# Kernel optimization log

Hardware: AMD Instinct MI355X
Metric: run time of the kernel (lower is better)

The kernel has to match this reference:

```python
import jax, jax.numpy as jnp
import numpy as np

B, H, S, D = 2, 8, 4096, 64

def setup_inputs() -> dict:
    key = jax.random.key(0)
    kq, kk, kv = jax.random.split(key, 3)
    queries = jax.random.normal(kq, (B, H, S, D), dtype=jnp.float32)
    keys = jax.random.normal(kk, (B, H, S, D), dtype=jnp.float32)
    values = jax.random.normal(kv, (B, H, S, D), dtype=jnp.float32)
    adj = jnp.zeros((1,), dtype=jnp.int32)  # unused by the module, kept for signature fidelity
    return {"queries": queries, "keys": keys, "values": values, "adj": adj}

def reference(queries, keys, values, adj):
    # scores: [B,H,S,S]; note the original divides by a hard-coded 16, not sqrt(d)
    scores = jnp.einsum('bhqd,bhkd->bhqk', queries, keys) / 16.0
    attn = jax.nn.softmax(scores, axis=-1)
    # dropout p=0.0 -> identity in eval/deterministic mode
    h = jnp.einsum('bhqk,bhkd->bhqd', attn, values)  # [B,H,S,D]
    # original uses .view (a reshape, NOT a transpose) to (S, B, H, D)
    return jnp.reshape(h, (S, B, H, D))
```

## Files before the change

kernel.cpp:

```cpp
#include <hip/hip_runtime.h>
#include <hip/hip_bf16.h>
#include <math.h>

#define S_LEN 4096
#define D_DIM 64
#define NBH   16
#define QPRE  0.09016844f

typedef __attribute__((ext_vector_type(8))) short bf16x8;
typedef __attribute__((ext_vector_type(4))) float f32x4;
typedef __attribute__((ext_vector_type(4))) __fp16 f16x4;
typedef __attribute__((ext_vector_type(2))) __fp16 f16x2;

__device__ __forceinline__ unsigned int pkbf(float lo, float hi) {
  unsigned int ua = __float_as_uint(lo) + 0x8000u;
  unsigned int ub = __float_as_uint(hi) + 0x8000u;
  return __builtin_amdgcn_perm(ub, ua, 0x07060302u);
}
__device__ __forceinline__ unsigned int pkhf(float lo, float hi) {
  f16x2 h = __builtin_amdgcn_cvt_pkrtz(lo, hi);
  return *(unsigned int*)&h;
}

__device__ __forceinline__ void dma16(const unsigned short* g, unsigned short* l) {
  __builtin_amdgcn_global_load_lds(
      (const __attribute__((address_space(1))) unsigned int*)g,
      (__attribute__((address_space(3))) unsigned int*)l, 16, 0, 0);
}

__global__ __launch_bounds__(256) void prep(const float* __restrict__ K,
                                            const float* __restrict__ V,
                                            unsigned short* __restrict__ Kbf,
                                            unsigned short* __restrict__ Vt) {
  const int bh = blockIdx.x >> 6;
  const int kt = blockIdx.x & 63;
  const int tid = threadIdx.x;

  const float* ks = K + ((size_t)bh * S_LEN + kt * 64) * D_DIM;
  unsigned short* kd = Kbf + ((size_t)bh * S_LEN + kt * 64) * D_DIM;
#pragma unroll
  for (int p = 0; p < 2; ++p) {
    int i = tid + p * 256;
    int row = i >> 3, c = (i & 7) * 8;
    float4 a = *(const float4*)&ks[row * D_DIM + c];
    float4 b = *(const float4*)&ks[row * D_DIM + c + 4];
    uint4 w;
    w.x = pkbf(a.x, a.y); w.y = pkbf(a.z, a.w);
    w.z = pkbf(b.x, b.y); w.w = pkbf(b.z, b.w);
    *(uint4*)&kd[row * D_DIM + c] = w;
  }

  __shared__ unsigned short tile[64][72];
  const float* src = V + ((size_t)bh * S_LEN + kt * 64) * D_DIM;
#pragma unroll
  for (int p = 0; p < 4; ++p) {
    int i = tid + p * 256;
    int row = i >> 4, c = (i & 15) * 4;
    float4 f = *(const float4*)&src[row * D_DIM + c];
    int cs = c ^ (((row >> 4) & 3) << 4);
    unsigned long long w = (unsigned long long)pkhf(f.x, f.y) |
                           ((unsigned long long)pkhf(f.z, f.w) << 32);
    *(unsigned long long*)&tile[row][cs] = w;
  }
  __syncthreads();
  const int d = tid >> 2, k0 = (tid & 3) * 16;
  unsigned short* dst = Vt + ((size_t)bh * D_DIM + d) * S_LEN + kt * 64 + k0;
  union { unsigned short u[16]; uint4 v[2]; } tmp;
  const int cr = d ^ k0;
#pragma unroll
  for (int i = 0; i < 16; ++i) tmp.u[i] = tile[k0 + i][cr];
  *(uint4*)&dst[0] = tmp.v[0];
  *(uint4*)&dst[8] = tmp.v[1];
}

__global__ __launch_bounds__(256) void fattn(const float* __restrict__ Q,
                                             const unsigned short* __restrict__ Kbf,
                                             const unsigned short* __restrict__ Vt,
                                             float* __restrict__ O) {
  const int bh   = blockIdx.x >> 5;
  const int qb   = blockIdx.x & 31;
  const int tid  = threadIdx.x;
  const int wave = tid >> 6;
  const int lane = tid & 63;
  const int quad = lane >> 4;
  const int l15  = lane & 15;
  const int rho  = l15 & 7;

  __shared__ unsigned short Ksh[2][64][64];
  __shared__ unsigned short Vsh[2][64][64];

  bf16x8 qf[2][2];
#pragma unroll
  for (int qt = 0; qt < 2; ++qt) {
    const int qg = qb * 128 + wave * 32 + qt * 16 + l15;
    const float* qp = Q + ((size_t)bh * S_LEN + qg) * D_DIM + quad * 8;
#pragma unroll
    for (int h = 0; h < 2; ++h) {
      float4 a = *(const float4*)&qp[h * 32];
      float4 b = *(const float4*)&qp[h * 32 + 4];
      union { unsigned int u[4]; bf16x8 v; } f;
      f.u[0] = pkbf(a.x * QPRE, a.y * QPRE);
      f.u[1] = pkbf(a.z * QPRE, a.w * QPRE);
      f.u[2] = pkbf(b.x * QPRE, b.y * QPRE);
      f.u[3] = pkbf(b.z * QPRE, b.w * QPRE);
      qf[qt][h] = f.v;
    }
  }

  f32x4 ot[2][4];
#pragma unroll
  for (int qt = 0; qt < 2; ++qt)
#pragma unroll
    for (int dt = 0; dt < 4; ++dt) ot[qt][dt] = (f32x4){0.f, 0.f, 0.f, 0.f};
  float Lp[2] = {0.f, 0.f};

  const unsigned short* Kb = Kbf + (size_t)bh * S_LEN * D_DIM;
  const unsigned short* Vb = Vt + (size_t)bh * D_DIM * S_LEN;

  const int r_lo = wave * 8 + (lane >> 3);
  const int csrc = ((lane & 7) ^ (lane >> 3)) * 8;

  const int ck0 = (quad ^ rho) * 8;
  const int ck1 = ((quad + 4) ^ rho) * 8;
  const int vrow  = l15 * 128 + (quad & 1) * 8;
  const int rho16 = rho << 4;
  const int vq2   = (quad >> 1) << 4;

#pragma unroll
  for (int c = 0; c < 2; ++c) {
    int r = r_lo + 32 * c;
    dma16(&Kb[(size_t)r * D_DIM + csrc], &Ksh[0][wave * 8 + 32 * c][0]);
    dma16(&Vb[(size_t)r * S_LEN + csrc], &Vsh[0][wave * 8 + 32 * c][0]);
  }

  for (int kt = 0; kt < 64; ++kt) {
    const int cur = kt & 1, nxt = cur ^ 1;
    __syncthreads();

    const int ktn = (kt + 1) & 63;
#pragma unroll
    for (int c = 0; c < 2; ++c) {
      int r = r_lo + 32 * c;
      dma16(&Kb[(size_t)(ktn * 64 + r) * D_DIM + csrc], &Ksh[nxt][wave * 8 + 32 * c][0]);
      dma16(&Vb[(size_t)r * S_LEN + ktn * 64 + csrc],   &Vsh[nxt][wave * 8 + 32 * c][0]);
    }

    unsigned int pfr[4][2][2];
#pragma unroll
    for (int mt = 0; mt < 4; ++mt) {
      const int row = mt * 16 + l15;
      bf16x8 kf0 = *(const bf16x8*)&Ksh[cur][row][ck0];
      bf16x8 kf1 = *(const bf16x8*)&Ksh[cur][row][ck1];
#pragma unroll
      for (int qt = 0; qt < 2; ++qt) {
        f32x4 acc = (f32x4){0.f, 0.f, 0.f, 0.f};
        acc = __builtin_amdgcn_mfma_f32_16x16x32_bf16(kf0, qf[qt][0], acc, 0, 0, 0);
        acc = __builtin_amdgcn_mfma_f32_16x16x32_bf16(kf1, qf[qt][1], acc, 0, 0, 0);
        float p0 = __builtin_amdgcn_exp2f(acc[0]);
        float p1 = __builtin_amdgcn_exp2f(acc[1]);
        float p2 = __builtin_amdgcn_exp2f(acc[2]);
        float p3 = __builtin_amdgcn_exp2f(acc[3]);
        Lp[qt] += (p0 + p1) + (p2 + p3);
        pfr[mt][qt][0] = pkhf(p0, p1);
        pfr[mt][qt][1] = pkhf(p2, p3);
      }
    }

    const char* vbase = (const char*)&Vsh[cur][0][0];
#pragma unroll
    for (int mt = 0; mt < 4; ++mt) {
      const int vb = vrow + (((mt << 5) + vq2) ^ rho16);
      union { unsigned int u[2]; f16x4 v; } pb0, pb1;
      pb0.u[0] = pfr[mt][0][0]; pb0.u[1] = pfr[mt][0][1];
      pb1.u[0] = pfr[mt][1][0]; pb1.u[1] = pfr[mt][1][1];
#pragma unroll
      for (int dt = 0; dt < 4; ++dt) {
        f16x4 va = *(const f16x4*)(vbase + vb + dt * 2048);
        ot[0][dt] = __builtin_amdgcn_mfma_f32_16x16x16f16(va, pb0.v, ot[0][dt], 0, 0, 0);
        ot[1][dt] = __builtin_amdgcn_mfma_f32_16x16x16f16(va, pb1.v, ot[1][dt], 0, 0, 0);
      }
    }
  }

#pragma unroll
  for (int qt = 0; qt < 2; ++qt) {
    float Lt = Lp[qt];
    Lt += __shfl_xor(Lt, 16);
    Lt += __shfl_xor(Lt, 32);
    float linv = 1.0f / Lt;
    const int qg = qb * 128 + wave * 32 + qt * 16 + l15;
    float* orow = O + ((size_t)bh * S_LEN + qg) * D_DIM;
#pragma unroll
    for (int dt = 0; dt < 4; ++dt) {
      float4 w;
      w.x = ot[qt][dt][0] * linv;
      w.y = ot[qt][dt][1] * linv;
      w.z = ot[qt][dt][2] * linv;
      w.w = ot[qt][dt][3] * linv;
      *(float4*)&orow[dt * 16 + quad * 4] = w;
    }
  }
}

extern "C" void kernel_launch(void* const* d_in, const int* in_sizes, int n_in,
                              void* d_out, int out_size, void* d_ws, size_t ws_size,
                              hipStream_t stream) {
  const float* Q = (const float*)d_in[0];
  const float* K = (const float*)d_in[1];
  const float* V = (const float*)d_in[2];
  unsigned short* Kbf = (unsigned short*)d_ws;
  unsigned short* Vt  = Kbf + (size_t)NBH * S_LEN * D_DIM;
  float* O = (float*)d_out;

  prep<<<NBH * (S_LEN / 64), 256, 0, stream>>>(K, V, Kbf, Vt);
  fattn<<<NBH * (S_LEN / 128), 256, 0, stream>>>(Q, Kbf, Vt, O);
}
```

Before: 199.7 us.

## Software-pipeline attention loop: overlap scores of next tile with PV of current

Restructures the main attention loop so the QK scores and exp for tile k+1 are computed while the PV products for tile k are issued, with a triple-buffered V tile and a prefetch distance of two. The row-sum of probabilities is computed with an extra MFMA against a ones vector instead of scalar adds and cross-lane shuffles. The prep kernel now issues all K and V loads up front and rewrites the V transpose store pattern. This costs extra LDS and registers (two probability buffers) and makes the row sums use the fp16-rounded probabilities.

```diff
diff --git a/kernel.cpp b/kernel.cpp
--- a/kernel.cpp
+++ b/kernel.cpp
@@ -35,42 +35,57 @@
   const int bh = blockIdx.x >> 6;
   const int kt = blockIdx.x & 63;
   const int tid = threadIdx.x;
-
+  __shared__ unsigned short tile[64][72];
+
+  const float* src = V + ((size_t)bh * S_LEN + kt * 64) * D_DIM;
+  float4 vf[4];
+#pragma unroll
+  for (int p = 0; p < 4; ++p) {
+    int i = tid + p * 256;
+    vf[p] = *(const float4*)&src[(i >> 4) * D_DIM + (i & 15) * 4];
+  }
   const float* ks = K + ((size_t)bh * S_LEN + kt * 64) * D_DIM;
+  float4 ka[4];
+#pragma unroll
+  for (int p = 0; p < 2; ++p) {
+    int i = tid + p * 256;
+    int row = i >> 3, c = (i & 7) * 8;
+    ka[2 * p]     = *(const float4*)&ks[row * D_DIM + c];
+    ka[2 * p + 1] = *(const float4*)&ks[row * D_DIM + c + 4];
+  }
+
+#pragma unroll
+  for (int p = 0; p < 4; ++p) {
+    int i = tid + p * 256;
+    int row = i >> 4, c = (i & 15) * 4;
+    int cs = c ^ (((row >> 4) & 3) << 4);
+    unsigned long long w = (unsigned long long)pkhf(vf[p].x, vf[p].y) |
+                           ((unsigned long long)pkhf(vf[p].z, vf[p].w) << 32);
+    *(unsigned long long*)&tile[row][cs] = w;
+  }
+  __syncthreads();
+
   unsigned short* kd = Kbf + ((size_t)bh * S_LEN + kt * 64) * D_DIM;
 #pragma unroll
   for (int p = 0; p < 2; ++p) {
     int i = tid + p * 256;
     int row = i >> 3, c = (i & 7) * 8;
-    float4 a = *(const float4*)&ks[row * D_DIM + c];
-    float4 b = *(const float4*)&ks[row * D_DIM + c + 4];
     uint4 w;
-    w.x = pkbf(a.x, a.y); w.y = pkbf(a.z, a.w);
-    w.z = pkbf(b.x, b.y); w.w = pkbf(b.z, b.w);
+    w.x = pkbf(ka[2 * p].x, ka[2 * p].y);     w.y = pkbf(ka[2 * p].z, ka[2 * p].w);
+    w.z = pkbf(ka[2 * p + 1].x, ka[2 * p + 1].y); w.w = pkbf(ka[2 * p + 1].z, ka[2 * p + 1].w);
     *(uint4*)&kd[row * D_DIM + c] = w;
   }
 
-  __shared__ unsigned short tile[64][72];
-  const float* src = V + ((size_t)bh * S_LEN + kt * 64) * D_DIM;
-#pragma unroll
-  for (int p = 0; p < 4; ++p) {
-    int i = tid + p * 256;
-    int row = i >> 4, c = (i & 15) * 4;
-    float4 f = *(const float4*)&src[row * D_DIM + c];
-    int cs = c ^ (((row >> 4) & 3) << 4);
-    unsigned long long w = (unsigned long long)pkhf(f.x, f.y) |
-                           ((unsigned long long)pkhf(f.z, f.w) << 32);
-    *(unsigned long long*)&tile[row][cs] = w;
-  }
-  __syncthreads();
-  const int d = tid >> 2, k0 = (tid & 3) * 16;
-  unsigned short* dst = Vt + ((size_t)bh * D_DIM + d) * S_LEN + kt * 64 + k0;
-  union { unsigned short u[16]; uint4 v[2]; } tmp;
-  const int cr = d ^ k0;
-#pragma unroll
-  for (int i = 0; i < 16; ++i) tmp.u[i] = tile[k0 + i][cr];
-  *(uint4*)&dst[0] = tmp.v[0];
-  *(uint4*)&dst[8] = tmp.v[1];
+  const int kc = tid & 7;
+#pragma unroll
+  for (int p = 0; p < 2; ++p) {
+    int d = p * 32 + (tid >> 3);
+    int col = d ^ (((kc >> 1) & 3) << 4);
+    union { unsigned short u[8]; uint4 v; } t;
+#pragma unroll
+    for (int i = 0; i < 8; ++i) t.u[i] = tile[kc * 8 + i][col];
+    *(uint4*)&Vt[((size_t)bh * D_DIM + d) * S_LEN + kt * 64 + kc * 8] = t.v;
+  }
 }
 
 __global__ __launch_bounds__(256) void fattn(const float* __restrict__ Q,
@@ -87,7 +102,7 @@
   const int rho  = l15 & 7;
 
   __shared__ unsigned short Ksh[2][64][64];
-  __shared__ unsigned short Vsh[2][64][64];
+  __shared__ unsigned short Vsh[3][64][64];
 
   bf16x8 qf[2][2];
 #pragma unroll
@@ -112,7 +127,8 @@
   for (int qt = 0; qt < 2; ++qt)
 #pragma unroll
     for (int dt = 0; dt < 4; ++dt) ot[qt][dt] = (f32x4){0.f, 0.f, 0.f, 0.f};
-  float Lp[2] = {0.f, 0.f};
+  f32x4 otL[2] = {(f32x4){0.f, 0.f, 0.f, 0.f}, (f32x4){0.f, 0.f, 0.f, 0.f}};
+  const f16x4 ones = (f16x4){(__fp16)1.0f, (__fp16)1.0f, (__fp16)1.0f, (__fp16)1.0f};
 
   const unsigned short* Kb = Kbf + (size_t)bh * S_LEN * D_DIM;
   const unsigned short* Vb = Vt + (size_t)bh * D_DIM * S_LEN;
@@ -126,68 +142,76 @@
   const int rho16 = rho << 4;
   const int vq2   = (quad >> 1) << 4;
 
-#pragma unroll
-  for (int c = 0; c < 2; ++c) {
-    int r = r_lo + 32 * c;
-    dma16(&Kb[(size_t)r * D_DIM + csrc], &Ksh[0][wave * 8 + 32 * c][0]);
-    dma16(&Vb[(size_t)r * S_LEN + csrc], &Vsh[0][wave * 8 + 32 * c][0]);
-  }
-
-  for (int kt = 0; kt < 64; ++kt) {
-    const int cur = kt & 1, nxt = cur ^ 1;
-    __syncthreads();
-
-    const int ktn = (kt + 1) & 63;
-#pragma unroll
-    for (int c = 0; c < 2; ++c) {
-      int r = r_lo + 32 * c;
-      dma16(&Kb[(size_t)(ktn * 64 + r) * D_DIM + csrc], &Ksh[nxt][wave * 8 + 32 * c][0]);
-      dma16(&Vb[(size_t)r * S_LEN + ktn * 64 + csrc],   &Vsh[nxt][wave * 8 + 32 * c][0]);
-    }
-
-    unsigned int pfr[4][2][2];
-#pragma unroll
-    for (int mt = 0; mt < 4; ++mt) {
-      const int row = mt * 16 + l15;
-      bf16x8 kf0 = *(const bf16x8*)&Ksh[cur][row][ck0];
-      bf16x8 kf1 = *(const bf16x8*)&Ksh[cur][row][ck1];
-#pragma unroll
-      for (int qt = 0; qt < 2; ++qt) {
-        f32x4 acc = (f32x4){0.f, 0.f, 0.f, 0.f};
-        acc = __builtin_amdgcn_mfma_f32_16x16x32_bf16(kf0, qf[qt][0], acc, 0, 0, 0);
-        acc = __builtin_amdgcn_mfma_f32_16x16x32_bf16(kf1, qf[qt][1], acc, 0, 0, 0);
-        float p0 = __builtin_amdgcn_exp2f(acc[0]);
-        float p1 = __builtin_amdgcn_exp2f(acc[1]);
-        float p2 = __builtin_amdgcn_exp2f(acc[2]);
-        float p3 = __builtin_amdgcn_exp2f(acc[3]);
-        Lp[qt] += (p0 + p1) + (p2 + p3);
-        pfr[mt][qt][0] = pkhf(p0, p1);
-        pfr[mt][qt][1] = pkhf(p2, p3);
-      }
-    }
-
-    const char* vbase = (const char*)&Vsh[cur][0][0];
-#pragma unroll
-    for (int mt = 0; mt < 4; ++mt) {
-      const int vb = vrow + (((mt << 5) + vq2) ^ rho16);
-      union { unsigned int u[2]; f16x4 v; } pb0, pb1;
-      pb0.u[0] = pfr[mt][0][0]; pb0.u[1] = pfr[mt][0][1];
-      pb1.u[0] = pfr[mt][1][0]; pb1.u[1] = pfr[mt][1][1];
-#pragma unroll
-      for (int dt = 0; dt < 4; ++dt) {
-        f16x4 va = *(const f16x4*)(vbase + vb + dt * 2048);
-        ot[0][dt] = __builtin_amdgcn_mfma_f32_16x16x16f16(va, pb0.v, ot[0][dt], 0, 0, 0);
-        ot[1][dt] = __builtin_amdgcn_mfma_f32_16x16x16f16(va, pb1.v, ot[1][dt], 0, 0, 0);
-      }
-    }
-  }
+#define DMAK(T, B) do { const int t_ = (T); \
+  dma16(&Kb[(size_t)(t_ * 64 + r_lo) * 64 + csrc],      &Ksh[B][wave * 8][0]); \
+  dma16(&Kb[(size_t)(t_ * 64 + r_lo + 32) * 64 + csrc], &Ksh[B][wave * 8 + 32][0]); } while (0)
+#define DMAV(T, B) do { const int t_ = (T); \
+  dma16(&Vb[(size_t)r_lo * S_LEN + t_ * 64 + csrc],        &Vsh[B][wave * 8][0]); \
+  dma16(&Vb[(size_t)(r_lo + 32) * S_LEN + t_ * 64 + csrc], &Vsh[B][wave * 8 + 32][0]); } while (0)
+
+#define SCORES(KB, PD) do { \
+  _Pragma("unroll") \
+  for (int mt = 0; mt < 4; ++mt) { \
+    const int row_ = mt * 16 + l15; \
+    bf16x8 kf0 = *(const bf16x8*)&Ksh[KB][row_][ck0]; \
+    bf16x8 kf1 = *(const bf16x8*)&Ksh[KB][row_][ck1]; \
+    _Pragma("unroll") \
+    for (int qt = 0; qt < 2; ++qt) { \
+      f32x4 acc = (f32x4){0.f, 0.f, 0.f, 0.f}; \
+      acc = __builtin_amdgcn_mfma_f32_16x16x32_bf16(kf0, qf[qt][0], acc, 0, 0, 0); \
+      acc = __builtin_amdgcn_mfma_f32_16x16x32_bf16(kf1, qf[qt][1], acc, 0, 0, 0); \
+      PD[mt][qt][0] = pkhf(__builtin_amdgcn_exp2f(acc[0]), __builtin_amdgcn_exp2f(acc[1])); \
+      PD[mt][qt][1] = pkhf(__builtin_amdgcn_exp2f(acc[2]), __builtin_amdgcn_exp2f(acc[3])); \
+    } \
+  } } while (0)
+
+#define PVSTEP(VB, PU) do { \
+  const char* vbase = (const char*)&Vsh[VB][0][0]; \
+  _Pragma("unroll") \
+  for (int mt = 0; mt < 4; ++mt) { \
+    const int vb_ = vrow + (((mt << 5) + vq2) ^ rho16); \
+    union { unsigned int u[2]; f16x4 v; } pb0, pb1; \
+    pb0.u[0] = PU[mt][0][0]; pb0.u[1] = PU[mt][0][1]; \
+    pb1.u[0] = PU[mt][1][0]; pb1.u[1] = PU[mt][1][1]; \
+    otL[0] = __builtin_amdgcn_mfma_f32_16x16x16f16(ones, pb0.v, otL[0], 0, 0, 0); \
+    otL[1] = __builtin_amdgcn_mfma_f32_16x16x16f16(ones, pb1.v, otL[1], 0, 0, 0); \
+    _Pragma("unroll") \
+    for (int dt = 0; dt < 4; ++dt) { \
+      f16x4 va = *(const f16x4*)(vbase + vb_ + dt * 2048); \
+      ot[0][dt] = __builtin_amdgcn_mfma_f32_16x16x16f16(va, pb0.v, ot[0][dt], 0, 0, 0); \
+      ot[1][dt] = __builtin_amdgcn_mfma_f32_16x16x16f16(va, pb1.v, ot[1][dt], 0, 0, 0); \
+    } \
+  } } while (0)
+
+#define ITER(KT, KBU, KBL, VBU, VBL, PU, PD) do { \
+  __syncthreads(); \
+  if ((KT) < 62) { DMAK((KT) + 2, KBL); DMAV((KT) + 2, VBL); } \
+  SCORES(KBU, PD); \
+  PVSTEP(VBU, PU); } while (0)
+
+  unsigned int pA[4][2][2], pB[4][2][2];
+
+  DMAK(0, 0); DMAV(0, 0);
+  __syncthreads();
+  SCORES(0, pA);
+  DMAK(1, 1); DMAV(1, 1);
+
+  for (int b = 0; b < 60; b += 6) {
+    ITER(b + 0, 1, 0, 0, 2, pA, pB);
+    ITER(b + 1, 0, 1, 1, 0, pB, pA);
+    ITER(b + 2, 1, 0, 2, 1, pA, pB);
+    ITER(b + 3, 0, 1, 0, 2, pB, pA);
+    ITER(b + 4, 1, 0, 1, 0, pA, pB);
+    ITER(b + 5, 0, 1, 2, 1, pB, pA);
+  }
+  ITER(60, 1, 0, 0, 2, pA, pB);
+  ITER(61, 0, 1, 1, 0, pB, pA);
+  ITER(62, 1, 0, 2, 1, pA, pB);
+  PVSTEP(0, pB);
 
 #pragma unroll
   for (int qt = 0; qt < 2; ++qt) {
-    float Lt = Lp[qt];
-    Lt += __shfl_xor(Lt, 16);
-    Lt += __shfl_xor(Lt, 32);
-    float linv = 1.0f / Lt;
+    float linv = 1.0f / otL[qt][0];
     const int qg = qb * 128 + wave * 32 + qt * 16 + l15;
     float* orow = O + ((size_t)bh * S_LEN + qg) * D_DIM;
 #pragma unroll
@@ -200,6 +224,11 @@
       *(float4*)&orow[dt * 16 + quad * 4] = w;
     }
   }
+#undef DMAK
+#undef DMAV
+#undef SCORES
+#undef PVSTEP
+#undef ITER
 }
 
 extern "C" void kernel_launch(void* const* d_in, const int* in_sizes, int n_in,
```

Result: faster. 190.1 us (-4.8%).
